# Optimization experiments

Measured on AMD Instinct MI355X. Metric: run time of the kernel, lower is better.

Reference implementation:

```python
import jax, jax.numpy as jnp
import numpy as np

B, S, DM = 4, 2048, 1024
H, HD = 16, 64  # num_heads, head_dimension


def setup_inputs() -> dict:
    key = jax.random.key(0)
    ks = jax.random.split(key, 11)
    s = 0.02
    return {
        "queries": jax.random.normal(ks[0], (B, S, DM), dtype=jnp.float32),
        "keys": jax.random.normal(ks[1], (B, S, DM), dtype=jnp.float32),
        "values": jax.random.normal(ks[2], (B, S, DM), dtype=jnp.float32),
        # projection params, stored [in, out] (transpose of torch Linear weight)
        "Wq": jax.random.normal(ks[3], (DM, H * HD), dtype=jnp.float32) * s,
        "bq": jnp.zeros((H * HD,), dtype=jnp.float32),
        "Wk": jax.random.normal(ks[4], (DM, H * HD), dtype=jnp.float32) * s,
        "bk": jnp.zeros((H * HD,), dtype=jnp.float32),
        "Wv": jax.random.normal(ks[5], (DM, H * HD), dtype=jnp.float32) * s,
        "bv": jnp.zeros((H * HD,), dtype=jnp.float32),
        "Wo": jax.random.normal(ks[6], (H * HD, DM), dtype=jnp.float32) * s,
        "bo": jnp.zeros((DM,), dtype=jnp.float32),
    }


def reference(queries, keys, values, Wq, bq, Wk, bk, Wv, bv, Wo, bo):
    b, s, _ = queries.shape
    # project and split heads: [b, s, H*HD] -> [b, H, s, HD]
    def split(x):
        return x.reshape(b, s, H, HD).transpose(0, 2, 1, 3)
    q = split(queries @ Wq + bq)
    k = split(keys @ Wk + bk)
    v = split(values @ Wv + bv)
    # raw scores [b, H, sq, sk]
    attn = jnp.einsum("bhqd,bhkd->bhqk", q, k)
    # FAITHFUL to source: mask is a no-op (masked_fill result discarded);
    # softmax over axis=2 (the QUERY axis), then scaled by 1/sqrt(HD) after.
    attn = jax.nn.softmax(attn, axis=2) / jnp.sqrt(jnp.float32(HD))
    out = jnp.einsum("bhqk,bhkd->bhqd", attn, v)  # [b, H, s, HD]
    out = out.transpose(0, 2, 1, 3).reshape(b, s, H * HD)
    return out @ Wo + bo
```

## Files before the change

kernel.cpp:

```cpp
#include <hip/hip_runtime.h>
#include <cstddef>


typedef unsigned short u16t;
typedef __attribute__((ext_vector_type(8))) short short8;
typedef __attribute__((ext_vector_type(4))) float floatx4;
typedef __attribute__((ext_vector_type(4))) unsigned int uintx4;

#define MFMA16(a, b, c) __builtin_amdgcn_mfma_f32_16x16x32_bf16((a), (b), (c), 0, 0, 0)
#define GLDS16(g, l)                                                        \
  __builtin_amdgcn_global_load_lds(                                         \
      (const __attribute__((address_space(1))) unsigned int*)(g),           \
      (__attribute__((address_space(3))) unsigned int*)(l), 16, 0, 0)

#if __has_builtin(__builtin_amdgcn_exp2f)
#define EXP2(x) __builtin_amdgcn_exp2f(x)
#else
#define EXP2(x) __expf(0.69314718f * (x))
#endif

static __device__ __forceinline__ u16t f2bf(float f) {
  union { float f; unsigned u; } v; v.f = f;
  unsigned r = v.u + 0x7FFFu + ((v.u >> 16) & 1u);
  return (u16t)(r >> 16);
}
static __device__ __forceinline__ unsigned pack2(float hi, float lo) {
  union { float f; unsigned u; } a, b; a.f = hi; b.f = lo;
  return __builtin_amdgcn_perm(a.u + 0x8000u, b.u + 0x8000u, 0x07060302u);
}

static __device__ __forceinline__ int swz(int row, int col) {
  return (((col >> 3) ^ (row & 7)) << 3) | (col & 7);
}

#define SEQ    2048
#define NHEAD  16
#define HDIM   64
#define DMODEL 1024

__global__ __launch_bounds__(256)
void wt_kernel(const float* __restrict__ W0, const float* __restrict__ W1,
               const float* __restrict__ W2, const float* __restrict__ W3,
               u16t* __restrict__ T0, u16t* __restrict__ T1,
               u16t* __restrict__ T2, u16t* __restrict__ T3) {
  int id = blockIdx.x * 256 + threadIdx.x;
  int wsel = id >> 17;
  int r = id & 131071;
  int n = r & 1023;
  int k0 = (r >> 10) << 3;
  const float* W = wsel == 0 ? W0 : wsel == 1 ? W1 : wsel == 2 ? W2 : W3;
  u16t* T = wsel == 0 ? T0 : wsel == 1 ? T1 : wsel == 2 ? T2 : T3;
  const float* src = W + (size_t)k0 * 1024 + n;
  float f[8];
#pragma unroll
  for (int i = 0; i < 8; ++i) f[i] = src[(size_t)i * 1024];
  uint4 p;
  p.x = pack2(f[1], f[0]); p.y = pack2(f[3], f[2]);
  p.z = pack2(f[5], f[4]); p.w = pack2(f[7], f[6]);
  *(uint4*)&T[(size_t)n * 1024 + (k0 & ~63) + swz(n, k0 & 63)] = p;
}

template <int MODE>
__global__ __launch_bounds__(256)
void gemm_bt(const void* __restrict__ Ap0, const void* __restrict__ Ap1,
             const u16t* __restrict__ BT0, const u16t* __restrict__ BT1,
             const float* __restrict__ bias0, const float* __restrict__ bias1,
             void* __restrict__ Cp0, void* __restrict__ Cp1,
             float sc0, float sc1, const float* __restrict__ sscv) {
  constexpr int K = 1024;
  __shared__ __align__(16) u16t lA[128 * 64];
  __shared__ __align__(16) u16t lB[128 * 64];
  const int z = blockIdx.z;
  const void* Ap = z ? Ap1 : Ap0;
  const u16t* BT = z ? BT1 : BT0;
  const float* bias = z ? bias1 : bias0;
  void* Cp = z ? Cp1 : Cp0;
  const float qsc = z ? sc1 : sc0;
  const int tid = threadIdx.x;
  const int lane = tid & 63, w = tid >> 6;
  const int wm = w >> 1, wn = w & 1;
  const int lrow = lane & 15, lq = lane >> 4;
  const int m0 = blockIdx.y * 128, n0 = blockIdx.x * 128;

  floatx4 acc[4][4];
#pragma unroll
  for (int i = 0; i < 4; ++i)
#pragma unroll
    for (int j = 0; j < 4; ++j) acc[i][j] = {0.f, 0.f, 0.f, 0.f};

  for (int kb = 0; kb < K; kb += 64) {
    if constexpr (MODE == 1) {
      const u16t* Ag = (const u16t*)Ap;
#pragma unroll
      for (int i = 0; i < 4; ++i) {
        int chunk = w * 4 + i;
        int off = chunk * 1024 + lane * 16;
        int r = off >> 7, ib = off & 127;
        GLDS16(Ag + (size_t)(m0 + r) * K + kb + (ib >> 1), &lA[chunk * 512]);
      }
    } else {
      const float* Ag = (const float*)Ap;
#pragma unroll
      for (int i = 0; i < 8; ++i) {
        int e = (i * 256 + tid) * 4;
        int r = e >> 6, c = e & 63;
        const float* src = Ag + (size_t)(m0 + r) * K + kb + c;
        uint2 p;
        p.x = pack2(src[1], src[0]);
        p.y = pack2(src[3], src[2]);
        *(uint2*)&lA[r * 64 + swz(r, c)] = p;
      }
    }
#pragma unroll
    for (int i = 0; i < 4; ++i) {
      int chunk = w * 4 + i;
      int off = chunk * 1024 + lane * 16;
      int r = off >> 7, ib = off & 127;
      GLDS16(BT + (size_t)(n0 + r) * K + kb + (ib >> 1), &lB[chunk * 512]);
    }
    __syncthreads();
#pragma unroll
    for (int kk = 0; kk < 2; ++kk) {
      short8 af[4], bfr[4];
#pragma unroll
      for (int t = 0; t < 4; ++t) {
        int ar = wm * 64 + t * 16 + lrow;
        af[t] = *(const short8*)&lA[ar * 64 + swz(ar, kk * 32 + lq * 8)];
      }
#pragma unroll
      for (int t = 0; t < 4; ++t) {
        int br = wn * 64 + t * 16 + lrow;
        bfr[t] = *(const short8*)&lB[br * 64 + swz(br, kk * 32 + lq * 8)];
      }
#pragma unroll
      for (int i = 0; i < 4; ++i)
#pragma unroll
        for (int j = 0; j < 4; ++j)
          acc[i][j] = MFMA16(af[i], bfr[j], acc[i][j]);
    }
    __syncthreads();
  }

  float bvv[4];
#pragma unroll
  for (int j = 0; j < 4; ++j) bvv[j] = bias[n0 + wn * 64 + j * 16 + lrow];
  const int h = (n0 + wn * 64) >> 6;
#pragma unroll
  for (int i = 0; i < 4; ++i) {
#pragma unroll
    for (int r = 0; r < 4; ++r) {
      int rg = m0 + wm * 64 + i * 16 + lq * 4 + r;
      int b = rg >> 11, s = rg & 2047;
      float rs;
      if constexpr (MODE == 2) rs = sscv[(size_t)(b * NHEAD + h) * SEQ + s];
      else                     rs = qsc;
#pragma unroll
      for (int j = 0; j < 4; ++j) {
        int cg = n0 + wn * 64 + j * 16 + lrow;
        float v = acc[i][j][r] + bvv[j];
        if constexpr (MODE == 1) {
          ((float*)Cp)[(size_t)rg * 1024 + cg] = v;
        } else {
          v *= rs;
          int d = cg & 63;
          size_t bh = (size_t)(b * NHEAD + h);
          if constexpr (MODE == 0) {
            ((u16t*)Cp)[(bh * SEQ + s) * HDIM + swz(s, d)] = f2bf(v);
          } else {
            int sp = (s & ~31) | (((s >> 2) & 3) << 3) | (s & 3) |
                     (((s >> 4) & 1) << 2);
            ((u16t*)Cp)[(bh * HDIM + d) * SEQ + (s & ~127) + swz(d, sp & 127)] =
                f2bf(v);
          }
        }
      }
    }
  }
}

__global__ __launch_bounds__(256)
void stats_kernel(const u16t* __restrict__ Qb, const u16t* __restrict__ Kb,
                  float* __restrict__ ss) {
  __shared__ __align__(16) u16t lK[128 * 64];
  __shared__ __align__(16) u16t lQ[128 * 64];
  const int tid = threadIdx.x, lane = tid & 63, w = tid >> 6;
  const int lrow = lane & 15, lq = lane >> 4;
  const int bh = blockIdx.x;
  const int c0 = blockIdx.y * 128;
  const u16t* Kbase = Kb + (size_t)bh * (SEQ * HDIM);
  const u16t* Qbase = Qb + (size_t)bh * (SEQ * HDIM);

#pragma unroll
  for (int i = 0; i < 4; ++i) {
    int chunk = w * 4 + i;
    GLDS16(Kbase + (size_t)c0 * HDIM + chunk * 512 + lane * 8, &lK[chunk * 512]);
  }

  short8 bfK[4];
  float lcur[2] = {0.f, 0.f};

  for (int q0 = 0; q0 < SEQ; q0 += 128) {
#pragma unroll
    for (int i = 0; i < 4; ++i) {
      int chunk = w * 4 + i;
      GLDS16(Qbase + (size_t)q0 * HDIM + chunk * 512 + lane * 8, &lQ[chunk * 512]);
    }
    __syncthreads();
    if (q0 == 0) {
#pragma unroll
      for (int nt = 0; nt < 2; ++nt) {
        int kr = w * 32 + nt * 16 + lrow;
        bfK[nt * 2]     = *(const short8*)&lK[kr * 64 + swz(kr, lq * 8)];
        bfK[nt * 2 + 1] = *(const short8*)&lK[kr * 64 + swz(kr, lq * 8 + 32)];
      }
    }
#pragma unroll
    for (int mt = 0; mt < 8; ++mt) {
      int qr = mt * 16 + lrow;
      short8 af0 = *(const short8*)&lQ[qr * 64 + swz(qr, lq * 8)];
      short8 af1 = *(const short8*)&lQ[qr * 64 + swz(qr, lq * 8 + 32)];
#pragma unroll
      for (int nt = 0; nt < 2; ++nt) {
        floatx4 a = {0.f, 0.f, 0.f, 0.f};
        a = MFMA16(af0, bfK[nt * 2], a);
        a = MFMA16(af1, bfK[nt * 2 + 1], a);
        lcur[nt] += EXP2(a[0]) + EXP2(a[1]) + EXP2(a[2]) + EXP2(a[3]);
      }
    }
    __syncthreads();
  }
#pragma unroll
  for (int t = 0; t < 2; ++t) {
    float ll = lcur[t];
    ll += __shfl_xor(ll, 16);
    ll += __shfl_xor(ll, 32);
    lcur[t] = ll;
  }
  if (lane < 16) {
#pragma unroll
    for (int t = 0; t < 2; ++t) {
      int col = c0 + w * 32 + t * 16 + lane;
      ss[(size_t)bh * SEQ + col] = 1.f / (8.f * lcur[t]);
    }
  }
}

__global__ __launch_bounds__(256)
void attn_kernel(const u16t* __restrict__ Qb, const u16t* __restrict__ Kb,
                 const u16t* __restrict__ Vt, u16t* __restrict__ Hout) {
  __shared__ __align__(16) u16t lK[128 * 64];
  __shared__ __align__(16) u16t lV[64 * 128];
  const int tid = threadIdx.x, lane = tid & 63, w = tid >> 6;
  const int lrow = lane & 15, lq = lane >> 4;
  const int bh = blockIdx.x, q0 = blockIdx.y * 128;
  const size_t hb = (size_t)bh * (SEQ * HDIM);

#pragma unroll
  for (int i = 0; i < 4; ++i) {
    int chunk = w * 4 + i;
    GLDS16(Qb + hb + (size_t)q0 * HDIM + chunk * 512 + lane * 8, &lK[chunk * 512]);
  }
  __syncthreads();
  short8 bq[2][2];
#pragma unroll
  for (int j = 0; j < 2; ++j) {
    int qr = w * 32 + j * 16 + lrow;
    bq[j][0] = *(const short8*)&lK[qr * 64 + swz(qr, lq * 8)];
    bq[j][1] = *(const short8*)&lK[qr * 64 + swz(qr, lq * 8 + 32)];
  }
  __syncthreads();

  floatx4 ao[2][4];
#pragma unroll
  for (int j = 0; j < 2; ++j)
#pragma unroll
    for (int t = 0; t < 4; ++t) ao[j][t] = {0.f, 0.f, 0.f, 0.f};

  for (int kt = 0; kt < 16; ++kt) {
    const int k0 = kt * 128;
#pragma unroll
    for (int i = 0; i < 4; ++i) {
      int chunk = w * 4 + i;
      GLDS16(Kb + hb + (size_t)k0 * HDIM + chunk * 512 + lane * 8, &lK[chunk * 512]);
    }
#pragma unroll
    for (int i = 0; i < 4; ++i) {
      int chunk = w * 4 + i;
      int off = chunk * 1024 + lane * 16;
      int d = off >> 8, ib = off & 255;
      GLDS16(Vt + hb + ((size_t)d << 11) + k0 + (ib >> 1), &lV[chunk * 512]);
    }
    __syncthreads();

#pragma unroll
    for (int kw = 0; kw < 4; ++kw) {
      short8 ak[2][2];
#pragma unroll
      for (int t = 0; t < 2; ++t) {
        int kr = (kw * 2 + t) * 16 + lrow;
        ak[t][0] = *(const short8*)&lK[kr * 64 + swz(kr, lq * 8)];
        ak[t][1] = *(const short8*)&lK[kr * 64 + swz(kr, lq * 8 + 32)];
      }
      short8 pa[2];
#pragma unroll
      for (int j = 0; j < 2; ++j) {
        floatx4 s0 = {0.f, 0.f, 0.f, 0.f}, s1 = {0.f, 0.f, 0.f, 0.f};
        s0 = MFMA16(ak[0][0], bq[j][0], s0);
        s0 = MFMA16(ak[0][1], bq[j][1], s0);
        s1 = MFMA16(ak[1][0], bq[j][0], s1);
        s1 = MFMA16(ak[1][1], bq[j][1], s1);
        uintx4 pw;
        pw[0] = pack2(EXP2(s0[1]), EXP2(s0[0]));
        pw[1] = pack2(EXP2(s0[3]), EXP2(s0[2]));
        pw[2] = pack2(EXP2(s1[1]), EXP2(s1[0]));
        pw[3] = pack2(EXP2(s1[3]), EXP2(s1[2]));
        pa[j] = __builtin_bit_cast(short8, pw);
      }
#pragma unroll
      for (int dt = 0; dt < 4; ++dt) {
        int vr = dt * 16 + lrow;
        short8 bv = *(const short8*)&lV[vr * 128 + swz(vr, kw * 32 + lq * 8)];
        ao[0][dt] = MFMA16(pa[0], bv, ao[0][dt]);
        ao[1][dt] = MFMA16(pa[1], bv, ao[1][dt]);
      }
    }
    __syncthreads();
  }

  const int b = bh >> 4, h = bh & 15;
#pragma unroll
  for (int j = 0; j < 2; ++j)
#pragma unroll
    for (int dt = 0; dt < 4; ++dt) {
      int d = dt * 16 + lrow;
#pragma unroll
      for (int r = 0; r < 4; ++r) {
        int q = q0 + w * 32 + j * 16 + lq * 4 + r;
        Hout[((size_t)b * SEQ + q) * DMODEL + h * HDIM + swz(q, d)] = f2bf(ao[j][dt][r]);
      }
    }
}

extern "C" void kernel_launch(void* const* d_in, const int* in_sizes, int n_in,
                              void* d_out, int out_size, void* d_ws, size_t ws_size,
                              hipStream_t stream) {
  (void)in_sizes; (void)n_in; (void)out_size; (void)ws_size;
  const float* queries = (const float*)d_in[0];
  const float* keys    = (const float*)d_in[1];
  const float* values  = (const float*)d_in[2];
  const float* Wq = (const float*)d_in[3];
  const float* bq = (const float*)d_in[4];
  const float* Wk = (const float*)d_in[5];
  const float* bk = (const float*)d_in[6];
  const float* Wv = (const float*)d_in[7];
  const float* bv = (const float*)d_in[8];
  const float* Wo = (const float*)d_in[9];
  const float* bo = (const float*)d_in[10];

  char* ws = (char*)d_ws;
  const size_t MB = 1024 * 1024;
  u16t* Qb   = (u16t*)(ws + 0 * MB);
  u16t* Kb   = (u16t*)(ws + 16 * MB);
  u16t* Vt   = (u16t*)(ws + 32 * MB);
  u16t* Hout = (u16t*)(ws + 48 * MB);
  u16t* wqt  = (u16t*)(ws + 64 * MB);
  u16t* wkt  = (u16t*)(ws + 66 * MB);
  u16t* wvt  = (u16t*)(ws + 68 * MB);
  u16t* wot  = (u16t*)(ws + 70 * MB);
  float* ssc = (float*)(ws + 72 * MB);

  wt_kernel<<<2048, 256, 0, stream>>>(Wq, Wk, Wv, Wo, wqt, wkt, wvt, wot);

  gemm_bt<0><<<dim3(8, 64, 2), 256, 0, stream>>>(
      queries, keys, wqt, wkt, bq, bk, Qb, Kb, 1.44269504f, 1.0f, nullptr);

  stats_kernel<<<dim3(64, 16), 256, 0, stream>>>(Qb, Kb, ssc);

  gemm_bt<2><<<dim3(8, 64, 1), 256, 0, stream>>>(
      values, values, wvt, wvt, bv, bv, Vt, Vt, 1.0f, 1.0f, ssc);

  attn_kernel<<<dim3(64, 16), 256, 0, stream>>>(Qb, Kb, Vt, Hout);

  gemm_bt<1><<<dim3(8, 64, 1), 256, 0, stream>>>(
      Hout, Hout, wot, wot, bo, bo, d_out, d_out, 1.0f, 1.0f, nullptr);
}
```

Before: 413.3 us.

## Pre-convert Q/K inputs to swizzled bf16 and remap GEMM tiles per XCD

Adds a separate conversion kernel that turns the fp32 query and key inputs into swizzled bf16 buffers. The Q/K projection GEMM can then load A tiles with direct global-to-LDS loads instead of doing per-thread fp32 loads and packing inside the K loop. It also remaps block indices so that consecutive blocks on the same XCD share M rows, aiming for better L2 reuse. The cost is an extra kernel launch and an extra read and write pass over 32 MB of inputs, and workspace buffers are now aliased (Hout with qcv, Vt with kcv).

```diff
diff --git a/kernel.cpp b/kernel.cpp
--- a/kernel.cpp
+++ b/kernel.cpp
@@ -58,6 +58,24 @@
   p.x = pack2(f[1], f[0]); p.y = pack2(f[3], f[2]);
   p.z = pack2(f[5], f[4]); p.w = pack2(f[7], f[6]);
   *(uint4*)&T[(size_t)n * 1024 + (k0 & ~63) + swz(n, k0 & 63)] = p;
+}
+
+__global__ __launch_bounds__(256)
+void cvt_kernel(const float* __restrict__ X0, const float* __restrict__ X1,
+                u16t* __restrict__ T0, u16t* __restrict__ T1) {
+  int id = blockIdx.x * 256 + threadIdx.x;
+  int wsel = id >> 20;
+  int r = id & 1048575;
+  int m = r >> 7;
+  int k0 = (r & 127) << 3;
+  const float* X = wsel == 0 ? X0 : X1;
+  u16t* T = wsel == 0 ? T0 : T1;
+  const float4* src = (const float4*)(X + (size_t)m * 1024 + k0);
+  float4 a = src[0], b = src[1];
+  uint4 p;
+  p.x = pack2(a.y, a.x); p.y = pack2(a.w, a.z);
+  p.z = pack2(b.y, b.x); p.w = pack2(b.w, b.z);
+  *(uint4*)&T[(size_t)m * 1024 + (k0 & ~63) + swz(m, k0 & 63)] = p;
 }
 
 template <int MODE>
@@ -80,7 +98,10 @@
   const int lane = tid & 63, w = tid >> 6;
   const int wm = w >> 1, wn = w & 1;
   const int lrow = lane & 15, lq = lane >> 4;
-  const int m0 = blockIdx.y * 128, n0 = blockIdx.x * 128;
+  const int raw = blockIdx.y * 8 + blockIdx.x;
+  const int xcd = raw & 7, slot = raw >> 3;
+  const int m0 = (xcd * 8 + (slot >> 3)) * 128;
+  const int n0 = (slot & 7) * 128;
 
   floatx4 acc[4][4];
 #pragma unroll
@@ -89,16 +110,7 @@
     for (int j = 0; j < 4; ++j) acc[i][j] = {0.f, 0.f, 0.f, 0.f};
 
   for (int kb = 0; kb < K; kb += 64) {
-    if constexpr (MODE == 1) {
-      const u16t* Ag = (const u16t*)Ap;
-#pragma unroll
-      for (int i = 0; i < 4; ++i) {
-        int chunk = w * 4 + i;
-        int off = chunk * 1024 + lane * 16;
-        int r = off >> 7, ib = off & 127;
-        GLDS16(Ag + (size_t)(m0 + r) * K + kb + (ib >> 1), &lA[chunk * 512]);
-      }
-    } else {
+    if constexpr (MODE == 2) {
       const float* Ag = (const float*)Ap;
 #pragma unroll
       for (int i = 0; i < 8; ++i) {
@@ -109,6 +121,15 @@
         p.x = pack2(src[1], src[0]);
         p.y = pack2(src[3], src[2]);
         *(uint2*)&lA[r * 64 + swz(r, c)] = p;
+      }
+    } else {
+      const u16t* Ag = (const u16t*)Ap;
+#pragma unroll
+      for (int i = 0; i < 4; ++i) {
+        int chunk = w * 4 + i;
+        int off = chunk * 1024 + lane * 16;
+        int r = off >> 7, ib = off & 127;
+        GLDS16(Ag + (size_t)(m0 + r) * K + kb + (ib >> 1), &lA[chunk * 512]);
       }
     }
 #pragma unroll
@@ -361,8 +382,10 @@
   const size_t MB = 1024 * 1024;
   u16t* Qb   = (u16t*)(ws + 0 * MB);
   u16t* Kb   = (u16t*)(ws + 16 * MB);
-  u16t* Vt   = (u16t*)(ws + 32 * MB);
-  u16t* Hout = (u16t*)(ws + 48 * MB);
+  u16t* qcv  = (u16t*)(ws + 32 * MB);
+  u16t* Hout = qcv;
+  u16t* kcv  = (u16t*)(ws + 48 * MB);
+  u16t* Vt   = kcv;
   u16t* wqt  = (u16t*)(ws + 64 * MB);
   u16t* wkt  = (u16t*)(ws + 66 * MB);
   u16t* wvt  = (u16t*)(ws + 68 * MB);
@@ -371,8 +394,10 @@
 
   wt_kernel<<<2048, 256, 0, stream>>>(Wq, Wk, Wv, Wo, wqt, wkt, wvt, wot);
 
+  cvt_kernel<<<8192, 256, 0, stream>>>(queries, keys, qcv, kcv);
+
   gemm_bt<0><<<dim3(8, 64, 2), 256, 0, stream>>>(
-      queries, keys, wqt, wkt, bq, bk, Qb, Kb, 1.44269504f, 1.0f, nullptr);
+      qcv, kcv, wqt, wkt, bq, bk, Qb, Kb, 1.44269504f, 1.0f, nullptr);
 
   stats_kernel<<<dim3(64, 16), 256, 0, stream>>>(Qb, Kb, ssc);
 
```

New measurement: 384.9 us. -6.9%, faster.
